# Kernel tuning notes

Measured on AMD Instinct MI355X. Metric: run time of the kernel, lower is better.

Reference implementation:

```python
import jax, jax.numpy as jnp
import numpy as np

B, S, NX, NH = 4, 2048, 1024, 16
HD = NX // NH
MASKED_BIAS = -10000.0


def setup_inputs() -> dict:
    key = jax.random.key(0)
    k1, k2, k3 = jax.random.split(key, 3)
    return {
        "hidden_states": jax.random.normal(k1, (B, S, NX), dtype=jnp.float32),
        "c_attn_w": jax.random.normal(k2, (NX, 3 * NX), dtype=jnp.float32) * 0.02,
        "c_attn_b": jnp.zeros((3 * NX,), dtype=jnp.float32),
        "c_proj_w": jax.random.normal(k3, (NX, NX), dtype=jnp.float32) * 0.02,
        "c_proj_b": jnp.zeros((NX,), dtype=jnp.float32),
    }


def reference(hidden_states, c_attn_w, c_attn_b, c_proj_w, c_proj_b):
    b, s, nx = hidden_states.shape
    # fused QKV projection (Conv1D == x @ W + b)
    qkv = hidden_states @ c_attn_w + c_attn_b          # [b, s, 3*nx]
    q, k, v = jnp.split(qkv, 3, axis=-1)
    # split heads -> [b, h, s, d]
    q = q.reshape(b, s, NH, HD).transpose(0, 2, 1, 3)
    k = k.reshape(b, s, NH, HD).transpose(0, 2, 1, 3)
    v = v.reshape(b, s, NH, HD).transpose(0, 2, 1, 3)
    # scaled scores [b, h, s, s]
    w = jnp.einsum("bhqd,bhkd->bhqk", q, k) / jnp.float32(np.sqrt(HD))
    # causal mask via torch.where(mask, w, -10000.0) semantics
    causal = jnp.tril(jnp.ones((s, s), dtype=bool))
    w = jnp.where(causal[None, None], w, jnp.float32(MASKED_BIAS))
    w = jax.nn.softmax(w, axis=-1)
    a = jnp.einsum("bhqk,bhkd->bhqd", w, v)            # [b, h, s, d]
    # merge heads
    a = a.transpose(0, 2, 1, 3).reshape(b, s, nx)
    # output projection
    return a @ c_proj_w + c_proj_b
```

## Files before the change

kernel.cpp:

```cpp
#include <hip/hip_runtime.h>


typedef __bf16 bf16_t;
typedef __bf16 bf16x8 __attribute__((ext_vector_type(8)));
typedef __bf16 bf16x4 __attribute__((ext_vector_type(4)));
typedef float  f32x4  __attribute__((ext_vector_type(4)));

#define DI __device__ __forceinline__

static constexpr int Bq = 4, Sq = 2048, NXq = 1024, NHq = 16, HDq = 64;

DI void gl2lds16(const void* g, void* l) {
#if defined(__has_builtin)
#if __has_builtin(__builtin_amdgcn_global_load_lds)
  __builtin_amdgcn_global_load_lds(
      (const __attribute__((address_space(1))) void*)g,
      (__attribute__((address_space(3))) void*)l, 16, 0, 0);
  return;
#endif
#endif
  *(bf16x8*)l = *(const bf16x8*)g;
}

DI float fast_exp2(float x) {
#if defined(__has_builtin)
#if __has_builtin(__builtin_amdgcn_exp2f)
  return __builtin_amdgcn_exp2f(x);
#else
  return exp2f(x);
#endif
#else
  return exp2f(x);
#endif
}

__global__ __launch_bounds__(256) void prep(
    const float* __restrict__ X, const float* __restrict__ W1,
    const float* __restrict__ W2, bf16_t* __restrict__ Xb,
    bf16_t* __restrict__ Wt1, bf16_t* __restrict__ Wt2) {
  __shared__ float t[32][33];
  const int id = blockIdx.x, tid = threadIdx.x;
  if (id < 2048) {
    const float* src = X + (size_t)id * 4096;
    bf16_t* dst = Xb + (size_t)id * 4096;
#pragma unroll
    for (int i = 0; i < 4; ++i) {
      float4 v = *(const float4*)(src + i * 1024 + tid * 4);
      bf16x4 o;
      o[0] = (bf16_t)v.x; o[1] = (bf16_t)v.y; o[2] = (bf16_t)v.z; o[3] = (bf16_t)v.w;
      *(bf16x4*)(dst + i * 1024 + tid * 4) = o;
    }
    return;
  }
  const float* in; bf16_t* out; int R, C, bx, by;
  if (id < 5120) {
    int tI = id - 2048; R = 1024; C = 3072; in = W1; out = Wt1;
    bx = (tI % 96) * 32; by = (tI / 96) * 32;
  } else {
    int tI = id - 5120; R = 1024; C = 1024; in = W2; out = Wt2;
    bx = (tI % 32) * 32; by = (tI / 32) * 32;
  }
  int tx = tid & 31, ty = tid >> 5;
#pragma unroll
  for (int i = 0; i < 32; i += 8)
    t[ty + i][tx] = in[(size_t)(by + ty + i) * C + bx + tx];
  __syncthreads();
#pragma unroll
  for (int i = 0; i < 32; i += 8)
    out[(size_t)(bx + ty + i) * R + by + tx] = (bf16_t)t[tx][ty + i];
}

DI void gemm_main(const bf16_t* __restrict__ A, const bf16_t* __restrict__ Bt,
                  int K, f32x4 acc[4][4], bf16_t* As, bf16_t* Bs,
                  int lane, int w) {
  const int wy = w >> 1, wx = w & 1;
  const int l15 = lane & 15, quad = lane >> 4;
  for (int kt = 0; kt < K; kt += 32) {
    __syncthreads();
#pragma unroll
    for (int i = 0; i < 2; ++i) {
      int g = w * 2 + i;
      int row = g * 16 + (lane >> 2);
      int ko = kt + (lane & 3) * 8;
      gl2lds16(A + (size_t)row * K + ko, As + g * 512 + lane * 8);
      gl2lds16(Bt + (size_t)row * K + ko, Bs + g * 512 + lane * 8);
    }
    __syncthreads();
    bf16x8 af[4], bfr[4];
#pragma unroll
    for (int mi = 0; mi < 4; ++mi)
      af[mi] = *(const bf16x8*)(As + (wy * 64 + mi * 16 + l15) * 32 + quad * 8);
#pragma unroll
    for (int ni = 0; ni < 4; ++ni)
      bfr[ni] = *(const bf16x8*)(Bs + (wx * 64 + ni * 16 + l15) * 32 + quad * 8);
#pragma unroll
    for (int mi = 0; mi < 4; ++mi)
#pragma unroll
      for (int ni = 0; ni < 4; ++ni)
        acc[mi][ni] = __builtin_amdgcn_mfma_f32_16x16x32_bf16(
            af[mi], bfr[ni], acc[mi][ni], 0, 0, 0);
  }
}

__global__ __launch_bounds__(256) void gemm_qkv(
    const bf16_t* __restrict__ X, const bf16_t* __restrict__ Wt,
    const float* __restrict__ bias, bf16_t* __restrict__ qw,
    bf16_t* __restrict__ kw, bf16_t* __restrict__ vtw) {
  __shared__ __align__(16) bf16_t As[128 * 32];
  __shared__ __align__(16) bf16_t Bs[128 * 32];
  const int tid = threadIdx.x, lane = tid & 63, w = tid >> 6;
  const int m0 = blockIdx.x * 128, n0 = blockIdx.y * 128;
  f32x4 acc[4][4];
#pragma unroll
  for (int mi = 0; mi < 4; ++mi)
#pragma unroll
    for (int ni = 0; ni < 4; ++ni) acc[mi][ni] = (f32x4){0.f, 0.f, 0.f, 0.f};
  gemm_main(X + (size_t)m0 * NXq, Wt + (size_t)n0 * NXq, NXq, acc, As, Bs, lane, w);

  const int wy = w >> 1, wx = w & 1, l15 = lane & 15, quad = lane >> 4;
  const float qscale = 0.125f * 1.44269504088896340736f;
#pragma unroll
  for (int mi = 0; mi < 4; ++mi) {
    int rowb = m0 + wy * 64 + mi * 16 + quad * 4;
    int bb = rowb >> 11, sl = rowb & 2047;
#pragma unroll
    for (int ni = 0; ni < 4; ++ni) {
      int col = n0 + wx * 64 + ni * 16 + l15;
      float bv = bias[col];
      f32x4 v = acc[mi][ni];
      int sec = col >> 10;
      int c = col & 1023;
      int h = c >> 6, d = c & 63;
      if (sec == 0) {
#pragma unroll
        for (int r = 0; r < 4; ++r)
          qw[(((size_t)bb * NHq + h) * Sq + sl + r) * HDq + d] =
              (bf16_t)((v[r] + bv) * qscale);
      } else if (sec == 1) {
#pragma unroll
        for (int r = 0; r < 4; ++r)
          kw[(((size_t)bb * NHq + h) * Sq + sl + r) * HDq + d] = (bf16_t)(v[r] + bv);
      } else {
        bf16x4 t;
#pragma unroll
        for (int r = 0; r < 4; ++r) t[r] = (bf16_t)(v[r] + bv);
        *(bf16x4*)(vtw + (((size_t)bb * NHq + h) * HDq + d) * Sq + sl) = t;
      }
    }
  }
}

__global__ __launch_bounds__(256, 4) void attn_fwd(
    const bf16_t* __restrict__ qw, const bf16_t* __restrict__ kw,
    const bf16_t* __restrict__ vtw, bf16_t* __restrict__ aw) {
  __shared__ __align__(16) bf16_t Ks[4096], Vs[4096];
  __shared__ __align__(16) bf16_t Ps[4][32 * 72];
  const int tid = threadIdx.x, lane = tid & 63, w = tid >> 6;
  const int l15 = lane & 15, quad = lane >> 4;

  const int id = blockIdx.x;
  const int bh = ((id & 7) << 3) | ((id >> 3) & 7);
  const int k4 = (id >> 6) & 3, quarter = id >> 8;
  int qtile;
  if (quarter == 0)      qtile = 15 - k4;
  else if (quarter == 1) qtile = 8 + k4;
  else if (quarter == 2) qtile = 7 - k4;
  else                   qtile = k4;
  const int b = bh >> 4, h = bh & 15;

  const bf16_t* Qg = qw + ((size_t)bh * Sq + qtile * 128) * HDq;
  const bf16_t* Kg = kw + (size_t)bh * Sq * HDq;
  const bf16_t* Vg = vtw + (size_t)bh * HDq * Sq;

  bf16x8 qf[2][2];
#pragma unroll
  for (int mi = 0; mi < 2; ++mi)
#pragma unroll
    for (int ks = 0; ks < 2; ++ks)
      qf[mi][ks] = *(const bf16x8*)(
          Qg + (size_t)((w * 2 + mi) * 16 + l15) * HDq + ks * 32 + quad * 8);

  f32x4 o[2][4];
  float lsum[2][4];
#pragma unroll
  for (int mi = 0; mi < 2; ++mi) {
#pragma unroll
    for (int dt = 0; dt < 4; ++dt) o[mi][dt] = (f32x4){0.f, 0.f, 0.f, 0.f};
#pragma unroll
    for (int r = 0; r < 4; ++r) lsum[mi][r] = 0.f;
  }

  bf16_t* Pw = &Ps[w][0];
  const int jmax = 2 * qtile + 2;
  for (int jt = 0; jt < jmax; ++jt) {
    __syncthreads();
#pragma unroll
    for (int i = 0; i < 2; ++i) {
      int u = w * 2 + i, p = u >> 2, g = u & 3;
      gl2lds16(Kg + (size_t)(jt * 64 + g * 16 + (lane >> 2)) * HDq + p * 32 + (lane & 3) * 8,
               Ks + u * 512 + lane * 8);
      gl2lds16(Vg + (size_t)(g * 16 + (lane >> 2)) * Sq + jt * 64 + p * 32 + (lane & 3) * 8,
               Vs + u * 512 + lane * 8);
    }
    __syncthreads();

    f32x4 sc[2][4];
#pragma unroll
    for (int mi = 0; mi < 2; ++mi)
#pragma unroll
      for (int nt = 0; nt < 4; ++nt) sc[mi][nt] = (f32x4){0.f, 0.f, 0.f, 0.f};
#pragma unroll
    for (int ks = 0; ks < 2; ++ks)
#pragma unroll
      for (int nt = 0; nt < 4; ++nt) {
        bf16x8 kf = *(const bf16x8*)(Ks + ks * 2048 + nt * 512 + (l15 * 4 + quad) * 8);
        sc[0][nt] = __builtin_amdgcn_mfma_f32_16x16x32_bf16(qf[0][ks], kf, sc[0][nt], 0, 0, 0);
        sc[1][nt] = __builtin_amdgcn_mfma_f32_16x16x32_bf16(qf[1][ks], kf, sc[1][nt], 0, 0, 0);
      }

    if (jt >= 2 * qtile) {
#pragma unroll
      for (int mi = 0; mi < 2; ++mi) {
        int qrow = qtile * 128 + (w * 2 + mi) * 16 + quad * 4;
#pragma unroll
        for (int nt = 0; nt < 4; ++nt) {
          int key = jt * 64 + nt * 16 + l15;
#pragma unroll
          for (int r = 0; r < 4; ++r)
            if (key > qrow + r) sc[mi][nt][r] = -1e30f;
        }
      }
    }

#pragma unroll
    for (int mi = 0; mi < 2; ++mi)
#pragma unroll
      for (int nt = 0; nt < 4; ++nt)
#pragma unroll
        for (int r = 0; r < 4; ++r) {
          float p = fast_exp2(sc[mi][nt][r]);
          lsum[mi][r] += p;
          Pw[(mi * 16 + quad * 4 + r) * 72 + nt * 16 + l15] = (bf16_t)p;
        }

#pragma unroll
    for (int kk = 0; kk < 2; ++kk) {
      bf16x8 ap0 = *(const bf16x8*)(Pw + (size_t)l15 * 72 + kk * 32 + quad * 8);
      bf16x8 ap1 = *(const bf16x8*)(Pw + (size_t)(16 + l15) * 72 + kk * 32 + quad * 8);
#pragma unroll
      for (int dt = 0; dt < 4; ++dt) {
        bf16x8 bv = *(const bf16x8*)(Vs + kk * 2048 + dt * 512 + (l15 * 4 + quad) * 8);
        o[0][dt] = __builtin_amdgcn_mfma_f32_16x16x32_bf16(ap0, bv, o[0][dt], 0, 0, 0);
        o[1][dt] = __builtin_amdgcn_mfma_f32_16x16x32_bf16(ap1, bv, o[1][dt], 0, 0, 0);
      }
    }
  }

  float linv[2][4];
#pragma unroll
  for (int mi = 0; mi < 2; ++mi)
#pragma unroll
    for (int r = 0; r < 4; ++r) {
      float s = lsum[mi][r];
#pragma unroll
      for (int off = 8; off > 0; off >>= 1) s += __shfl_xor(s, off);
      linv[mi][r] = 1.f / s;
    }

#pragma unroll
  for (int mi = 0; mi < 2; ++mi) {
    int s0 = qtile * 128 + (w * 2 + mi) * 16 + quad * 4;
#pragma unroll
    for (int dt = 0; dt < 4; ++dt) {
      int col = h * 64 + dt * 16 + l15;
#pragma unroll
      for (int r = 0; r < 4; ++r)
        aw[((size_t)b * Sq + s0 + r) * NXq + col] = (bf16_t)(o[mi][dt][r] * linv[mi][r]);
    }
  }
}

__global__ __launch_bounds__(256) void gemm_proj(
    const bf16_t* __restrict__ Aa, const bf16_t* __restrict__ Wt,
    const float* __restrict__ bias, float* __restrict__ out) {
  __shared__ __align__(16) bf16_t As[128 * 32];
  __shared__ __align__(16) bf16_t Bs[128 * 32];
  const int tid = threadIdx.x, lane = tid & 63, w = tid >> 6;
  const int m0 = blockIdx.x * 128, n0 = blockIdx.y * 128;
  f32x4 acc[4][4];
#pragma unroll
  for (int mi = 0; mi < 4; ++mi)
#pragma unroll
    for (int ni = 0; ni < 4; ++ni) acc[mi][ni] = (f32x4){0.f, 0.f, 0.f, 0.f};
  gemm_main(Aa + (size_t)m0 * NXq, Wt + (size_t)n0 * NXq, NXq, acc, As, Bs, lane, w);

  const int wy = w >> 1, wx = w & 1, l15 = lane & 15, quad = lane >> 4;
#pragma unroll
  for (int mi = 0; mi < 4; ++mi) {
    int rowb = m0 + wy * 64 + mi * 16 + quad * 4;
#pragma unroll
    for (int ni = 0; ni < 4; ++ni) {
      int col = n0 + wx * 64 + ni * 16 + l15;
      float bv = bias[col];
#pragma unroll
      for (int r = 0; r < 4; ++r)
        out[(size_t)(rowb + r) * NXq + col] = acc[mi][ni][r] + bv;
    }
  }
}

extern "C" void kernel_launch(void* const* d_in, const int* in_sizes, int n_in,
                              void* d_out, int out_size, void* d_ws, size_t ws_size,
                              hipStream_t stream) {
  const float* hidden   = (const float*)d_in[0];
  const float* c_attn_w = (const float*)d_in[1];
  const float* c_attn_b = (const float*)d_in[2];
  const float* c_proj_w = (const float*)d_in[3];
  const float* c_proj_b = (const float*)d_in[4];
  float* out = (float*)d_out;

  char* ws = (char*)d_ws;
  const size_t szX   = (size_t)8192 * 1024 * 2;
  const size_t szW1  = (size_t)3072 * 1024 * 2;
  const size_t szW2  = (size_t)1024 * 1024 * 2;
  const size_t szQKV = (size_t)Bq * NHq * Sq * HDq * 2;
  bf16_t* Xb  = (bf16_t*)(ws);
  bf16_t* Wt1 = (bf16_t*)(ws + szX);
  bf16_t* Wt2 = (bf16_t*)(ws + szX + szW1);
  bf16_t* qwp = (bf16_t*)(ws + szX + szW1 + szW2);
  bf16_t* kwp = (bf16_t*)(ws + szX + szW1 + szW2 + szQKV);
  bf16_t* vtp = (bf16_t*)(ws + szX + szW1 + szW2 + 2 * szQKV);
  bf16_t* awp = (bf16_t*)(ws + szX + szW1 + szW2 + 3 * szQKV);
  if (ws_size < szX + szW1 + szW2 + 4 * szQKV) return;

  prep<<<dim3(6144), dim3(256), 0, stream>>>(hidden, c_attn_w, c_proj_w,
                                             Xb, Wt1, Wt2);
  gemm_qkv<<<dim3(64, 24), dim3(256), 0, stream>>>(
      Xb, Wt1, c_attn_b, qwp, kwp, vtp);
  attn_fwd<<<dim3(1024), dim3(256), 0, stream>>>(qwp, kwp, vtp, awp);
  gemm_proj<<<dim3(64, 8), dim3(256), 0, stream>>>(
      awp, Wt2, c_proj_b, out);
}
```

Baseline: 247.2 us.

## Double-buffer K/V tiles in attention with 256-row Q tiles; narrow proj GEMM tiles

The attention kernel now handles 256 query rows per block (64 per wave) and double-buffers K/V tiles in LDS, prefetching the next tile before computing the current one. This halves redundant K/V loads and overlaps global-to-LDS transfers with MFMA work. Waves skip key tiles that lie entirely past their causal diagonal. Occupancy drops to 2 blocks per CU and the grid shrinks to 512 blocks, which risks load imbalance. The projection GEMM switches to 128x64 tiles with its own inline loop, doubling the block count to improve CU fill.

```diff
diff --git a/kernel.cpp b/kernel.cpp
--- a/kernel.cpp
+++ b/kernel.cpp
@@ -150,40 +150,45 @@
   }
 }
 
-__global__ __launch_bounds__(256, 4) void attn_fwd(
+__global__ __launch_bounds__(256, 2) void attn_fwd(
     const bf16_t* __restrict__ qw, const bf16_t* __restrict__ kw,
     const bf16_t* __restrict__ vtw, bf16_t* __restrict__ aw) {
-  __shared__ __align__(16) bf16_t Ks[4096], Vs[4096];
-  __shared__ __align__(16) bf16_t Ps[4][32 * 72];
+  __shared__ __align__(16) bf16_t Ks[2][4096], Vs[2][4096];
+  __shared__ __align__(16) bf16_t Ps[4][64 * 72];
   const int tid = threadIdx.x, lane = tid & 63, w = tid >> 6;
   const int l15 = lane & 15, quad = lane >> 4;
 
   const int id = blockIdx.x;
   const int bh = ((id & 7) << 3) | ((id >> 3) & 7);
-  const int k4 = (id >> 6) & 3, quarter = id >> 8;
-  int qtile;
-  if (quarter == 0)      qtile = 15 - k4;
-  else if (quarter == 1) qtile = 8 + k4;
-  else if (quarter == 2) qtile = 7 - k4;
-  else                   qtile = k4;
+  const int g = (id >> 6) & 3, half = id >> 8;
+  const int qtile = half ? g : 7 - g;
   const int b = bh >> 4, h = bh & 15;
 
-  const bf16_t* Qg = qw + ((size_t)bh * Sq + qtile * 128) * HDq;
+  const bf16_t* Qg = qw + ((size_t)bh * Sq + qtile * 256) * HDq;
   const bf16_t* Kg = kw + (size_t)bh * Sq * HDq;
   const bf16_t* Vg = vtw + (size_t)bh * HDq * Sq;
 
-  bf16x8 qf[2][2];
-#pragma unroll
-  for (int mi = 0; mi < 2; ++mi)
+  const int su = w * 2, sr = lane >> 2, sk = (lane & 3) * 8;
+
+#pragma unroll
+  for (int i = 0; i < 2; ++i) {
+    int u = su + i, p = u >> 2, gg = u & 3;
+    gl2lds16(Kg + (size_t)(gg * 16 + sr) * HDq + p * 32 + sk, Ks[0] + u * 512 + lane * 8);
+    gl2lds16(Vg + (size_t)(gg * 16 + sr) * Sq + p * 32 + sk, Vs[0] + u * 512 + lane * 8);
+  }
+
+  bf16x8 qf[4][2];
+#pragma unroll
+  for (int mi = 0; mi < 4; ++mi)
 #pragma unroll
     for (int ks = 0; ks < 2; ++ks)
       qf[mi][ks] = *(const bf16x8*)(
-          Qg + (size_t)((w * 2 + mi) * 16 + l15) * HDq + ks * 32 + quad * 8);
-
-  f32x4 o[2][4];
-  float lsum[2][4];
-#pragma unroll
-  for (int mi = 0; mi < 2; ++mi) {
+          Qg + (size_t)(w * 64 + mi * 16 + l15) * HDq + ks * 32 + quad * 8);
+
+  f32x4 o[4][4];
+  float lsum[4][4];
+#pragma unroll
+  for (int mi = 0; mi < 4; ++mi) {
 #pragma unroll
     for (int dt = 0; dt < 4; ++dt) o[mi][dt] = (f32x4){0.f, 0.f, 0.f, 0.f};
 #pragma unroll
@@ -191,91 +196,102 @@
   }
 
   bf16_t* Pw = &Ps[w][0];
-  const int jmax = 2 * qtile + 2;
+  const int jmax = 4 * qtile + 4;
+  const int jlast = 4 * qtile + w;
   for (int jt = 0; jt < jmax; ++jt) {
-    __syncthreads();
-#pragma unroll
-    for (int i = 0; i < 2; ++i) {
-      int u = w * 2 + i, p = u >> 2, g = u & 3;
-      gl2lds16(Kg + (size_t)(jt * 64 + g * 16 + (lane >> 2)) * HDq + p * 32 + (lane & 3) * 8,
-               Ks + u * 512 + lane * 8);
-      gl2lds16(Vg + (size_t)(g * 16 + (lane >> 2)) * Sq + jt * 64 + p * 32 + (lane & 3) * 8,
-               Vs + u * 512 + lane * 8);
-    }
-    __syncthreads();
-
-    f32x4 sc[2][4];
-#pragma unroll
-    for (int mi = 0; mi < 2; ++mi)
-#pragma unroll
-      for (int nt = 0; nt < 4; ++nt) sc[mi][nt] = (f32x4){0.f, 0.f, 0.f, 0.f};
+    const int cur = jt & 1;
+    __syncthreads();
+
+    if (jt + 1 < jmax) {
+      const int nxt = cur ^ 1;
+#pragma unroll
+      for (int i = 0; i < 2; ++i) {
+        int u = su + i, p = u >> 2, gg = u & 3;
+        gl2lds16(Kg + (size_t)((jt + 1) * 64 + gg * 16 + sr) * HDq + p * 32 + sk,
+                 Ks[nxt] + u * 512 + lane * 8);
+        gl2lds16(Vg + (size_t)(gg * 16 + sr) * Sq + (jt + 1) * 64 + p * 32 + sk,
+                 Vs[nxt] + u * 512 + lane * 8);
+      }
+    }
+
+    if (jt > jlast) continue;
+
+    const bf16_t* Kc = Ks[cur];
+    const bf16_t* Vc = Vs[cur];
+    const bool diag = (jt == jlast) && (w == (jt & 3) || jt == 4 * qtile + w);
+
+    bf16x8 kf[2][4];
 #pragma unroll
     for (int ks = 0; ks < 2; ++ks)
 #pragma unroll
-      for (int nt = 0; nt < 4; ++nt) {
-        bf16x8 kf = *(const bf16x8*)(Ks + ks * 2048 + nt * 512 + (l15 * 4 + quad) * 8);
-        sc[0][nt] = __builtin_amdgcn_mfma_f32_16x16x32_bf16(qf[0][ks], kf, sc[0][nt], 0, 0, 0);
-        sc[1][nt] = __builtin_amdgcn_mfma_f32_16x16x32_bf16(qf[1][ks], kf, sc[1][nt], 0, 0, 0);
-      }
-
-    if (jt >= 2 * qtile) {
-#pragma unroll
-      for (int mi = 0; mi < 2; ++mi) {
-        int qrow = qtile * 128 + (w * 2 + mi) * 16 + quad * 4;
+      for (int nt = 0; nt < 4; ++nt)
+        kf[ks][nt] = *(const bf16x8*)(Kc + (ks * 4 + nt) * 512 + (l15 * 4 + quad) * 8);
+
+#pragma unroll
+    for (int mi = 0; mi < 4; ++mi) {
+      f32x4 sc[4];
+#pragma unroll
+      for (int nt = 0; nt < 4; ++nt) sc[nt] = (f32x4){0.f, 0.f, 0.f, 0.f};
+#pragma unroll
+      for (int ks = 0; ks < 2; ++ks)
+#pragma unroll
+        for (int nt = 0; nt < 4; ++nt)
+          sc[nt] = __builtin_amdgcn_mfma_f32_16x16x32_bf16(qf[mi][ks], kf[ks][nt],
+                                                           sc[nt], 0, 0, 0);
+      if (diag) {
+        int qrow = qtile * 256 + w * 64 + mi * 16 + quad * 4;
 #pragma unroll
         for (int nt = 0; nt < 4; ++nt) {
           int key = jt * 64 + nt * 16 + l15;
 #pragma unroll
           for (int r = 0; r < 4; ++r)
-            if (key > qrow + r) sc[mi][nt][r] = -1e30f;
+            if (key > qrow + r) sc[nt][r] = -1e30f;
         }
       }
-    }
-
-#pragma unroll
-    for (int mi = 0; mi < 2; ++mi)
 #pragma unroll
       for (int nt = 0; nt < 4; ++nt)
 #pragma unroll
         for (int r = 0; r < 4; ++r) {
-          float p = fast_exp2(sc[mi][nt][r]);
+          float p = fast_exp2(sc[nt][r]);
           lsum[mi][r] += p;
           Pw[(mi * 16 + quad * 4 + r) * 72 + nt * 16 + l15] = (bf16_t)p;
         }
+    }
 
 #pragma unroll
     for (int kk = 0; kk < 2; ++kk) {
-      bf16x8 ap0 = *(const bf16x8*)(Pw + (size_t)l15 * 72 + kk * 32 + quad * 8);
-      bf16x8 ap1 = *(const bf16x8*)(Pw + (size_t)(16 + l15) * 72 + kk * 32 + quad * 8);
+      bf16x8 ap[4];
+#pragma unroll
+      for (int mi = 0; mi < 4; ++mi)
+        ap[mi] = *(const bf16x8*)(Pw + (size_t)(mi * 16 + l15) * 72 + kk * 32 + quad * 8);
 #pragma unroll
       for (int dt = 0; dt < 4; ++dt) {
-        bf16x8 bv = *(const bf16x8*)(Vs + kk * 2048 + dt * 512 + (l15 * 4 + quad) * 8);
-        o[0][dt] = __builtin_amdgcn_mfma_f32_16x16x32_bf16(ap0, bv, o[0][dt], 0, 0, 0);
-        o[1][dt] = __builtin_amdgcn_mfma_f32_16x16x32_bf16(ap1, bv, o[1][dt], 0, 0, 0);
+        bf16x8 bv = *(const bf16x8*)(Vc + (kk * 4 + dt) * 512 + (l15 * 4 + quad) * 8);
+#pragma unroll
+        for (int mi = 0; mi < 4; ++mi)
+          o[mi][dt] = __builtin_amdgcn_mfma_f32_16x16x32_bf16(ap[mi], bv,
+                                                              o[mi][dt], 0, 0, 0);
       }
     }
   }
 
-  float linv[2][4];
-#pragma unroll
-  for (int mi = 0; mi < 2; ++mi)
+#pragma unroll
+  for (int mi = 0; mi < 4; ++mi) {
+    float linv[4];
 #pragma unroll
     for (int r = 0; r < 4; ++r) {
       float s = lsum[mi][r];
 #pragma unroll
       for (int off = 8; off > 0; off >>= 1) s += __shfl_xor(s, off);
-      linv[mi][r] = 1.f / s;
-    }
-
-#pragma unroll
-  for (int mi = 0; mi < 2; ++mi) {
-    int s0 = qtile * 128 + (w * 2 + mi) * 16 + quad * 4;
+      linv[r] = 1.f / s;
+    }
+    int s0 = qtile * 256 + w * 64 + mi * 16 + quad * 4;
 #pragma unroll
     for (int dt = 0; dt < 4; ++dt) {
       int col = h * 64 + dt * 16 + l15;
 #pragma unroll
       for (int r = 0; r < 4; ++r)
-        aw[((size_t)b * Sq + s0 + r) * NXq + col] = (bf16_t)(o[mi][dt][r] * linv[mi][r]);
+        aw[((size_t)b * Sq + s0 + r) * NXq + col] = (bf16_t)(o[mi][dt][r] * linv[r]);
     }
   }
 }
@@ -284,23 +300,50 @@
     const bf16_t* __restrict__ Aa, const bf16_t* __restrict__ Wt,
     const float* __restrict__ bias, float* __restrict__ out) {
   __shared__ __align__(16) bf16_t As[128 * 32];
-  __shared__ __align__(16) bf16_t Bs[128 * 32];
+  __shared__ __align__(16) bf16_t Bs[64 * 32];
   const int tid = threadIdx.x, lane = tid & 63, w = tid >> 6;
-  const int m0 = blockIdx.x * 128, n0 = blockIdx.y * 128;
-  f32x4 acc[4][4];
+  const int m0 = blockIdx.x * 128, n0 = blockIdx.y * 64;
+  const int wy = w >> 1, wx = w & 1;
+  const int l15 = lane & 15, quad = lane >> 4;
+  const int sr = lane >> 2, sk = (lane & 3) * 8;
+  f32x4 acc[4][2];
 #pragma unroll
   for (int mi = 0; mi < 4; ++mi)
 #pragma unroll
-    for (int ni = 0; ni < 4; ++ni) acc[mi][ni] = (f32x4){0.f, 0.f, 0.f, 0.f};
-  gemm_main(Aa + (size_t)m0 * NXq, Wt + (size_t)n0 * NXq, NXq, acc, As, Bs, lane, w);
-
-  const int wy = w >> 1, wx = w & 1, l15 = lane & 15, quad = lane >> 4;
+    for (int ni = 0; ni < 2; ++ni) acc[mi][ni] = (f32x4){0.f, 0.f, 0.f, 0.f};
+
+  const bf16_t* A = Aa + (size_t)m0 * NXq;
+  const bf16_t* Bt = Wt + (size_t)n0 * NXq;
+  for (int kt = 0; kt < NXq; kt += 32) {
+    __syncthreads();
+#pragma unroll
+    for (int i = 0; i < 2; ++i) {
+      int gA = w * 2 + i;
+      gl2lds16(A + (size_t)(gA * 16 + sr) * NXq + kt + sk, As + gA * 512 + lane * 8);
+    }
+    gl2lds16(Bt + (size_t)(w * 16 + sr) * NXq + kt + sk, Bs + w * 512 + lane * 8);
+    __syncthreads();
+    bf16x8 af[4], bfr[2];
+#pragma unroll
+    for (int mi = 0; mi < 4; ++mi)
+      af[mi] = *(const bf16x8*)(As + (wy * 4 + mi) * 512 + l15 * 32 + quad * 8);
+#pragma unroll
+    for (int ni = 0; ni < 2; ++ni)
+      bfr[ni] = *(const bf16x8*)(Bs + (wx * 2 + ni) * 512 + l15 * 32 + quad * 8);
+#pragma unroll
+    for (int mi = 0; mi < 4; ++mi)
+#pragma unroll
+      for (int ni = 0; ni < 2; ++ni)
+        acc[mi][ni] = __builtin_amdgcn_mfma_f32_16x16x32_bf16(
+            af[mi], bfr[ni], acc[mi][ni], 0, 0, 0);
+  }
+
 #pragma unroll
   for (int mi = 0; mi < 4; ++mi) {
     int rowb = m0 + wy * 64 + mi * 16 + quad * 4;
 #pragma unroll
-    for (int ni = 0; ni < 4; ++ni) {
-      int col = n0 + wx * 64 + ni * 16 + l15;
+    for (int ni = 0; ni < 2; ++ni) {
+      int col = n0 + wx * 32 + ni * 16 + l15;
       float bv = bias[col];
 #pragma unroll
       for (int r = 0; r < 4; ++r)
@@ -337,7 +380,7 @@
                                              Xb, Wt1, Wt2);
   gemm_qkv<<<dim3(64, 24), dim3(256), 0, stream>>>(
       Xb, Wt1, c_attn_b, qwp, kwp, vtp);
-  attn_fwd<<<dim3(1024), dim3(256), 0, stream>>>(qwp, kwp, vtp, awp);
-  gemm_proj<<<dim3(64, 8), dim3(256), 0, stream>>>(
+  attn_fwd<<<dim3(512), dim3(256), 0, stream>>>(qwp, kwp, vtp, awp);
+  gemm_proj<<<dim3(64, 16), dim3(256), 0, stream>>>(
       awp, Wt2, c_proj_b, out);
 }
```

Result: slower. 258.4 us (+4.5%).
